# Kernel optimization log

Measured on AMD Instinct MI355X. Metric: run time of the kernel, lower is better.

The kernel has to match this reference:

```python
import jax, jax.numpy as jnp
import numpy as np

D_VOCAB, D_MODEL, N_CTX, D_MLP, D_HEAD, N_HEADS, N_LAYERS = 32000, 1024, 2048, 4096, 64, 16, 4
BATCH, SEQ = 2, 2048


def setup_inputs() -> dict:
    key = jax.random.key(0)
    ks = jax.random.split(key, 12)
    sd = 1.0 / np.sqrt(D_MODEL)
    inp = {
        'tokens': jax.random.randint(ks[0], (BATCH, SEQ), 0, D_VOCAB),
        'W_E': jax.random.normal(ks[1], (D_MODEL, D_VOCAB), jnp.float32) * sd,
        'W_pos': jax.random.normal(ks[2], (N_CTX, D_MODEL), jnp.float32) * sd,
        'W_K': jax.random.normal(ks[3], (N_LAYERS, N_HEADS, D_HEAD, D_MODEL), jnp.float32) * sd,
        'W_Q': jax.random.normal(ks[4], (N_LAYERS, N_HEADS, D_HEAD, D_MODEL), jnp.float32) * sd,
        'W_V': jax.random.normal(ks[5], (N_LAYERS, N_HEADS, D_HEAD, D_MODEL), jnp.float32) * sd,
        'W_O': jax.random.normal(ks[6], (N_LAYERS, D_MODEL, D_HEAD * N_HEADS), jnp.float32) * sd,
        'W_in': jax.random.normal(ks[7], (N_LAYERS, D_MLP, D_MODEL), jnp.float32) * sd,
        'b_in': jnp.zeros((N_LAYERS, D_MLP), jnp.float32),
        'W_out': jax.random.normal(ks[8], (N_LAYERS, D_MODEL, D_MLP), jnp.float32) * sd,
        'b_out': jnp.zeros((N_LAYERS, D_MODEL), jnp.float32),
        'W_U': jax.random.normal(ks[9], (D_MODEL, D_VOCAB), jnp.float32) / np.sqrt(D_VOCAB),
    }
    return inp


def reference(tokens, W_E, W_pos, W_K, W_Q, W_V, W_O, W_in, b_in, W_out, b_out, W_U):
    P = tokens.shape[-1]
    # Embed: einsum('dbp->bpd', W_E[:, x])  ==  W_E.T[tokens]
    x = W_E.T[tokens]                      # [b, p, d]
    x = x + W_pos[:P]                      # PosEmbed
    causal = jnp.tril(jnp.ones((P, P), dtype=bool))  # mask[q, p]: p <= q
    scale = 1.0 / np.sqrt(D_HEAD)
    for l in range(N_LAYERS):
        # --- Attention ---
        k = jnp.einsum('ihd,bpd->biph', W_K[l], x)
        q = jnp.einsum('ihd,bpd->biph', W_Q[l], x)
        v = jnp.einsum('ihd,bpd->biph', W_V[l], x)
        scores = jnp.einsum('biph,biqh->biqp', k, q)
        # tril(scores) - 1e10*(1-mask)  ==  where(mask, scores, -1e10)
        masked = jnp.where(causal, scores, jnp.float32(-1e10))
        attn = jax.nn.softmax(masked * scale, axis=-1)   # softmax over keys p
        z = jnp.einsum('biph,biqp->biqh', v, attn)       # [b, i, q, h]
        z_flat = jnp.transpose(z, (0, 2, 1, 3)).reshape(z.shape[0], P, -1)  # b q (i h)
        attn_out = jnp.einsum('df,bqf->bqd', W_O[l], z_flat)
        x = x + attn_out
        # --- MLP (ReLU) ---
        pre = jnp.einsum('md,bpd->bpm', W_in[l], x) + b_in[l]
        post = jax.nn.relu(pre)
        x = x + jnp.einsum('dm,bpm->bpd', W_out[l], post) + b_out[l]
    return x @ W_U                          # logits [b, p, d_vocab]
```

## Files before the change

### kernel.cpp

```cpp
#include <hip/hip_runtime.h>
#include <hip/hip_bf16.h>
#include <math.h>

#define DV   32000
#define DM   1024
#define DMLP 4096
#define DH   64
#define NH   16
#define NL   4
#define BATCH 2
#define S    2048
#define MTOK (BATCH*S)

typedef __bf16 bf16_t;
typedef bf16_t bf16x8 __attribute__((ext_vector_type(8)));
typedef float  f32x4  __attribute__((ext_vector_type(4)));

#define AS1 __attribute__((address_space(1)))
#define AS3 __attribute__((address_space(3)))

__device__ __forceinline__ void gload16(const bf16_t* g, bf16_t* l) {
    __builtin_amdgcn_global_load_lds((const AS1 void*)g, (AS3 void*)l, 16, 0, 0);
}

__device__ __forceinline__ unsigned short bfbits(float v) {
    union { bf16_t b; unsigned short u; } c; c.b = (bf16_t)v; return c.u;
}
__device__ __forceinline__ float b2f(unsigned short u) {
    union { float f; unsigned v; } c; c.v = ((unsigned)u) << 16; return c.f;
}

template<int MODE, bool BIAS, bool RELU>
__global__ __launch_bounds__(256, 2)
void gemm128d(const bf16_t* __restrict__ A, const bf16_t* __restrict__ Bm,
              char* __restrict__ Out, int ldc,
              const float* __restrict__ bias,
              float* __restrict__ resid, bf16_t* __restrict__ residb,
              int K)
{
    const int mb = blockIdx.x, nb = blockIdx.y;

    __shared__ alignas(16) bf16_t lds[2][2][128*64];

    const int tid  = threadIdx.x;
    const int wave = tid >> 6, lane = tid & 63;
    const int wm = wave >> 1, wn = wave & 1;
    const int l16 = lane & 15, lh = lane >> 4;

    const bf16_t* Abase = A  + (long)(mb*128)*K;
    const bf16_t* Bbase = Bm + (long)(nb*128)*K;

    auto stage2 = [&](int buf, int k0) {
#pragma unroll
        for (int mat=0; mat<2; ++mat) {
            const bf16_t* src = (mat ? Bbase : Abase) + k0;
            bf16_t* dst = &lds[buf][mat][0];
#pragma unroll
            for (int u=0; u<4; ++u) {
                int c = u*256 + tid;
                int row = c >> 3, lc = (c & 7) ^ (row & 7);
                gload16(&src[(long)row*K + lc*8], dst + c*8);
            }
        }
    };

    f32x4 acc[4][4];
#pragma unroll
    for (int i=0;i<4;i++)
#pragma unroll
        for (int j=0;j<4;j++) { f32x4 zv={0.f,0.f,0.f,0.f}; acc[i][j]=zv; }

    const int NT = K >> 6;
    stage2(0, 0);

    int cur = 0;
    for (int kt = 0; kt < NT; ++kt) {
        const int nxt = cur ^ 1;
        const bool more = (kt+1 < NT);

        if (more) {
            stage2(nxt, (kt+1) << 6);
            asm volatile("s_waitcnt vmcnt(8)" ::: "memory");
        } else {
            asm volatile("s_waitcnt vmcnt(0)" ::: "memory");
        }
        asm volatile("s_barrier" ::: "memory");

        bf16x8 af[4][2], bfr[4][2];
#pragma unroll
        for (int i=0;i<4;i++) {
            int ra = wm*64 + i*16 + l16;
#pragma unroll
            for (int kk=0;kk<2;kk++)
                af[i][kk] = *(const bf16x8*)&lds[cur][0][ra*64 + (((kk*4+lh)^(ra&7))*8)];
        }
#pragma unroll
        for (int j=0;j<2;j++) {
            int rb = wn*64 + j*16 + l16;
#pragma unroll
            for (int kk=0;kk<2;kk++)
                bfr[j][kk] = *(const bf16x8*)&lds[cur][1][rb*64 + (((kk*4+lh)^(rb&7))*8)];
        }
        __builtin_amdgcn_s_setprio(1);
#pragma unroll
        for (int kk=0;kk<2;kk++)
#pragma unroll
            for (int i=0;i<4;i++)
#pragma unroll
                for (int j=0;j<2;j++)
                    acc[i][j] = __builtin_amdgcn_mfma_f32_16x16x32_bf16(af[i][kk], bfr[j][kk], acc[i][j], 0,0,0);
        __builtin_amdgcn_s_setprio(0);

#pragma unroll
        for (int j=2;j<4;j++) {
            int rb = wn*64 + j*16 + l16;
#pragma unroll
            for (int kk=0;kk<2;kk++)
                bfr[j][kk] = *(const bf16x8*)&lds[cur][1][rb*64 + (((kk*4+lh)^(rb&7))*8)];
        }
        __builtin_amdgcn_s_setprio(1);
#pragma unroll
        for (int kk=0;kk<2;kk++)
#pragma unroll
            for (int i=0;i<4;i++)
#pragma unroll
                for (int j=2;j<4;j++)
                    acc[i][j] = __builtin_amdgcn_mfma_f32_16x16x32_bf16(af[i][kk], bfr[j][kk], acc[i][j], 0,0,0);
        __builtin_amdgcn_s_setprio(0);

        asm volatile("s_barrier" ::: "memory");
        cur = nxt;
    }

    if constexpr (MODE == 1) {
        float* lsl = reinterpret_cast<float*>(&lds[0][0][0]) + wave*(32*68);
        const int lrow = lane >> 4;
        const int lcq  = lane & 15;
#pragma unroll
        for (int ch=0; ch<2; ++ch) {
#pragma unroll
            for (int il=0; il<2; ++il)
#pragma unroll
                for (int j=0;j<4;j++)
#pragma unroll
                    for (int r=0;r<4;r++)
                        lsl[(il*16 + lh*4 + r)*68 + j*16 + l16] = acc[ch*2+il][j][r];
#pragma unroll
            for (int u=0; u<8; ++u) {
                int rl = u*4 + lrow;
                f32x4 v = *(const f32x4*)&lsl[rl*68 + lcq*4];
                long row = mb*128 + wm*64 + ch*32 + rl;
                long col = nb*128 + wn*64 + lcq*4;
                __builtin_nontemporal_store(v, (f32x4*)&((float*)Out)[row*ldc + col]);
            }
        }
    } else {
#pragma unroll
        for (int i=0;i<4;i++) {
            int row0 = mb*128 + wm*64 + i*16 + lh*4;
#pragma unroll
            for (int j=0;j<4;j++) {
                int col = nb*128 + wn*64 + j*16 + l16;
                float bv = BIAS ? bias[col] : 0.0f;
#pragma unroll
                for (int r=0;r<4;r++) {
                    int row = row0 + r;
                    float v = acc[i][j][r] + bv;
                    if (RELU) v = v > 0.f ? v : 0.f;
                    if constexpr (MODE == 0) {
                        ((bf16_t*)Out)[(long)row*ldc + col] = (bf16_t)v;
                    } else {
                        long o2 = (long)row*ldc + col;
                        float nv = resid[o2] + v;
                        resid[o2]  = nv;
                        residb[o2] = (bf16_t)nv;
                    }
                }
            }
        }
    }
}

template<int MODE, bool BIAS, bool RELU>
__global__ __launch_bounds__(512, 1)
void gemm256(const bf16_t* __restrict__ A, const bf16_t* __restrict__ Bm,
             char* __restrict__ Out, int ldc,
             const float* __restrict__ bias, int K)
{
    const int mb = blockIdx.x, nb = blockIdx.y;

    __shared__ alignas(16) bf16_t lds[2][2][2][128*64];

    const int tid  = threadIdx.x;
    const int wave = tid >> 6, lane = tid & 63;
    const int wm = wave >> 2, wn = wave & 3;
    const int l16 = lane & 15, lh = lane >> 4;

    const bf16_t* Abase = A  + (long)(mb*256)*K;
    const bf16_t* Bbase = Bm + (long)(nb*256)*K;

    const int c0 = tid,       r0 = c0 >> 3, lc0 = (c0 & 7) ^ (r0 & 7);
    const int c1 = 512 + tid, r1 = c1 >> 3, lc1 = (c1 & 7) ^ (r1 & 7);

    auto stage4 = [&](int buf, int k0) {
#pragma unroll
        for (int mat=0; mat<2; ++mat)
#pragma unroll
            for (int half=0; half<2; ++half) {
                const bf16_t* src = (mat ? Bbase : Abase) + (long)(half*128)*K + k0;
                bf16_t* dst = &lds[buf][mat][half][0];
                gload16(&src[(long)r0*K + lc0*8], dst + c0*8);
                gload16(&src[(long)r1*K + lc1*8], dst + c1*8);
            }
    };

    f32x4 acc[8][4];
#pragma unroll
    for (int i=0;i<8;i++)
#pragma unroll
        for (int j=0;j<4;j++) { f32x4 zv={0.f,0.f,0.f,0.f}; acc[i][j]=zv; }

    const int NT = K >> 6;
    stage4(0, 0);

    int cur = 0;
    for (int kt = 0; kt < NT; ++kt) {
        const int nxt = cur ^ 1;
        const bool more = (kt+1 < NT);

        if (more) {
            stage4(nxt, (kt+1) << 6);
            asm volatile("s_waitcnt vmcnt(8)" ::: "memory");
        } else {
            asm volatile("s_waitcnt vmcnt(0)" ::: "memory");
        }
        asm volatile("s_barrier" ::: "memory");

        bf16x8 af[4][2], bfr[4][2];
#pragma unroll
        for (int i=0;i<4;i++) {
            int ra = i*16 + l16;
#pragma unroll
            for (int kk=0;kk<2;kk++)
                af[i][kk] = *(const bf16x8*)&lds[cur][0][wm][ra*64 + (((kk*4+lh)^(ra&7))*8)];
        }
#pragma unroll
        for (int j=0;j<2;j++) {
            int rb = (wn&1)*64 + j*16 + l16;
#pragma unroll
            for (int kk=0;kk<2;kk++)
                bfr[j][kk] = *(const bf16x8*)&lds[cur][1][wn>>1][rb*64 + (((kk*4+lh)^(rb&7))*8)];
        }
        __builtin_amdgcn_s_setprio(1);
#pragma unroll
        for (int kk=0;kk<2;kk++)
#pragma unroll
            for (int i=0;i<4;i++)
#pragma unroll
                for (int j=0;j<2;j++)
                    acc[i][j] = __builtin_amdgcn_mfma_f32_16x16x32_bf16(af[i][kk], bfr[j][kk], acc[i][j], 0,0,0);
        __builtin_amdgcn_s_setprio(0);

#pragma unroll
        for (int j=2;j<4;j++) {
            int rb = (wn&1)*64 + j*16 + l16;
#pragma unroll
            for (int kk=0;kk<2;kk++)
                bfr[j][kk] = *(const bf16x8*)&lds[cur][1][wn>>1][rb*64 + (((kk*4+lh)^(rb&7))*8)];
        }
        __builtin_amdgcn_s_setprio(1);
#pragma unroll
        for (int kk=0;kk<2;kk++)
#pragma unroll
            for (int i=0;i<4;i++)
#pragma unroll
                for (int j=2;j<4;j++)
                    acc[i][j] = __builtin_amdgcn_mfma_f32_16x16x32_bf16(af[i][kk], bfr[j][kk], acc[i][j], 0,0,0);
        __builtin_amdgcn_s_setprio(0);

#pragma unroll
        for (int i=0;i<4;i++) {
            int ra = (i+4)*16 + l16;
#pragma unroll
            for (int kk=0;kk<2;kk++)
                af[i][kk] = *(const bf16x8*)&lds[cur][0][wm][ra*64 + (((kk*4+lh)^(ra&7))*8)];
        }
        __builtin_amdgcn_s_setprio(1);
#pragma unroll
        for (int kk=0;kk<2;kk++)
#pragma unroll
            for (int i=0;i<4;i++)
#pragma unroll
                for (int j=0;j<2;j++)
                    acc[i+4][j] = __builtin_amdgcn_mfma_f32_16x16x32_bf16(af[i][kk], bfr[j][kk], acc[i+4][j], 0,0,0);
        __builtin_amdgcn_s_setprio(0);

        __builtin_amdgcn_s_setprio(1);
#pragma unroll
        for (int kk=0;kk<2;kk++)
#pragma unroll
            for (int i=0;i<4;i++)
#pragma unroll
                for (int j=2;j<4;j++)
                    acc[i+4][j] = __builtin_amdgcn_mfma_f32_16x16x32_bf16(af[i][kk], bfr[j][kk], acc[i+4][j], 0,0,0);
        __builtin_amdgcn_s_setprio(0);

        asm volatile("s_barrier" ::: "memory");
        cur = nxt;
    }

    if constexpr (MODE == 1) {
        float* lsl = reinterpret_cast<float*>(&lds[0][0][0][0]) + wave*(32*68);
        const int lrow = lane >> 4;
        const int lcq  = lane & 15;
#pragma unroll
        for (int ch=0; ch<4; ++ch) {
#pragma unroll
            for (int il=0; il<2; ++il)
#pragma unroll
                for (int j=0;j<4;j++)
#pragma unroll
                    for (int r=0;r<4;r++)
                        lsl[(il*16 + lh*4 + r)*68 + j*16 + l16] = acc[ch*2+il][j][r];
#pragma unroll
            for (int u=0; u<8; ++u) {
                int rl = u*4 + lrow;
                f32x4 v = *(const f32x4*)&lsl[rl*68 + lcq*4];
                long row = mb*256 + wm*128 + ch*32 + rl;
                long col = nb*256 + wn*64 + lcq*4;
                __builtin_nontemporal_store(v, (f32x4*)&((float*)Out)[row*ldc + col]);
            }
        }
    } else {
#pragma unroll
        for (int i=0;i<8;i++) {
            int row0 = mb*256 + wm*128 + i*16 + lh*4;
#pragma unroll
            for (int j=0;j<4;j++) {
                int col = nb*256 + wn*64 + j*16 + l16;
                float bv = BIAS ? bias[col] : 0.0f;
#pragma unroll
                for (int r=0;r<4;r++) {
                    int row = row0 + r;
                    float v = acc[i][j][r] + bv;
                    if (RELU) v = v > 0.f ? v : 0.f;
                    ((bf16_t*)Out)[(long)row*ldc + col] = (bf16_t)v;
                }
            }
        }
    }
}

__global__ __launch_bounds__(256)
void flash_attn(const bf16_t* __restrict__ qkvf,
                const bf16_t* __restrict__ vtg,
                bf16_t* __restrict__ zf)
{
    const int bh = blockIdx.y;
    const int b  = bh >> 4, hd = bh & 15;

    __shared__ alignas(16) bf16_t Kl[2][64*64];
    __shared__ alignas(16) bf16_t Vtl[2][64*64];
    __shared__ alignas(16) bf16_t Pl[4*32*64];

    const int tid = threadIdx.x;
    const int wave = tid >> 6, lane = tid & 63;
    const int l16 = lane & 15, lh = lane >> 4;
    bf16_t* Pw = Pl + wave*32*64;

    auto stageKV = [&](int buf, int kv0) {
#pragma unroll
        for (int u=0; u<2; ++u) {
            int c = u*256 + tid;
            int row = c >> 3, lc = (c & 7) ^ (row & 7);
            gload16(&qkvf[((long)b*S + kv0 + row)*3072 + 1024 + hd*64 + lc*8], &Kl[buf][c*8]);
        }
#pragma unroll
        for (int u=0; u<2; ++u) {
            int c = u*256 + tid;
            int row = c >> 3, lc = (c & 7) ^ (row & 7);
            gload16(&vtg[((long)bh*DH + row)*S + kv0 + lc*8], &Vtl[buf][c*8]);
        }
    };

    const float C = 0.125f;

#pragma unroll 1
    for (int pass = 0; pass < 2; ++pass) {
        const int qt = pass == 0 ? (int)blockIdx.x : 15 - (int)blockIdx.x;
        const int wq_lo = qt*128 + wave*32;

        bf16x8 qr[2][2];
#pragma unroll
        for (int qf=0; qf<2; qf++) {
            int qg = wq_lo + qf*16 + l16;
#pragma unroll
            for (int dhh=0; dhh<2; dhh++)
                qr[qf][dhh] = *(const bf16x8*)&qkvf[((long)b*S + qg)*3072 + hd*64 + dhh*32 + lh*8];
        }

        f32x4 o[4][2];
#pragma unroll
        for (int d=0; d<4; d++)
#pragma unroll
            for (int qf=0; qf<2; qf++) { f32x4 zv={0.f,0.f,0.f,0.f}; o[d][qf]=zv; }
        float mrun[2] = {-1e30f, -1e30f};
        float lrun[2] = {0.f, 0.f};

        const int nt = 2*(qt+1);

        __syncthreads();
        stageKV(0, 0);
        int cur = 0;
        for (int t = 0; t < nt; ++t) {
            const int nxt = cur ^ 1;
            const bool more = (t+1 < nt);
            if (more) {
                stageKV(nxt, (t+1)*64);
                asm volatile("s_waitcnt vmcnt(4)" ::: "memory");
            } else {
                asm volatile("s_waitcnt vmcnt(0)" ::: "memory");
            }
            asm volatile("s_barrier" ::: "memory");

            const int kv0 = t*64;
            f32x4 s[4][2];
#pragma unroll
            for (int f=0; f<4; f++)
#pragma unroll
                for (int qf=0; qf<2; qf++) { f32x4 zv={0.f,0.f,0.f,0.f}; s[f][qf]=zv; }
            __builtin_amdgcn_s_setprio(1);
#pragma unroll
            for (int f=0; f<4; f++) {
                int krow = f*16 + l16;
#pragma unroll
                for (int dhh=0; dhh<2; dhh++) {
                    bf16x8 kfr = *(const bf16x8*)&Kl[cur][krow*64 + (((dhh*4+lh) ^ (krow&7))*8)];
#pragma unroll
                    for (int qf=0; qf<2; qf++)
                        s[f][qf] = __builtin_amdgcn_mfma_f32_16x16x32_bf16(kfr, qr[qf][dhh], s[f][qf], 0,0,0);
                }
            }
            __builtin_amdgcn_s_setprio(0);

            const bool needmask = (kv0 + 64 > wq_lo);

#pragma unroll
            for (int qf=0; qf<2; qf++) {
                int qg = wq_lo + qf*16 + l16;
                float pmax = -1e30f;
#pragma unroll
                for (int f=0; f<4; f++)
#pragma unroll
                    for (int r=0; r<4; r++) {
                        float sv = s[f][qf][r];
                        if (needmask && (kv0 + f*16 + lh*4 + r > qg)) { sv = -1e30f; s[f][qf][r] = sv; }
                        pmax = fmaxf(pmax, sv);
                    }
                pmax = fmaxf(pmax, __shfl_xor(pmax, 16));
                pmax = fmaxf(pmax, __shfl_xor(pmax, 32));
                float mnew = fmaxf(mrun[qf], pmax);
                float corr = __expf((mrun[qf] - mnew)*C);
                mrun[qf] = mnew;
                lrun[qf] *= corr;
#pragma unroll
                for (int d=0; d<4; d++) o[d][qf] *= corr;
                float lsum = 0.f;
                int qloc = qf*16 + l16;
#pragma unroll
                for (int f=0; f<4; f++) {
                    ushort4 pk;
                    float p0 = __expf((s[f][qf][0]-mnew)*C);
                    float p1 = __expf((s[f][qf][1]-mnew)*C);
                    float p2 = __expf((s[f][qf][2]-mnew)*C);
                    float p3 = __expf((s[f][qf][3]-mnew)*C);
                    lsum += (p0+p1) + (p2+p3);
                    pk.x = bfbits(p0); pk.y = bfbits(p1); pk.z = bfbits(p2); pk.w = bfbits(p3);
                    int phys = (f*2 + (lh>>1)) ^ (qloc & 7);
                    *(ushort4*)&Pw[qloc*64 + phys*8 + (lh&1)*4] = pk;
                }
                lrun[qf] += lsum;
            }

#pragma unroll
            for (int kh=0; kh<2; kh++) {
                bf16x8 pb[2];
#pragma unroll
                for (int qf=0; qf<2; qf++) {
                    int qloc = qf*16 + l16;
                    pb[qf] = *(const bf16x8*)&Pw[qloc*64 + (((kh*4+lh) ^ (qloc&7))*8)];
                }
                __builtin_amdgcn_s_setprio(1);
#pragma unroll
                for (int d=0; d<4; d++) {
                    int vrow = d*16 + l16;
                    bf16x8 va = *(const bf16x8*)&Vtl[cur][vrow*64 + (((kh*4+lh) ^ (vrow&7))*8)];
#pragma unroll
                    for (int qf=0; qf<2; qf++)
                        o[d][qf] = __builtin_amdgcn_mfma_f32_16x16x32_bf16(va, pb[qf], o[d][qf], 0,0,0);
                }
                __builtin_amdgcn_s_setprio(0);
            }
            asm volatile("s_barrier" ::: "memory");
            cur = nxt;
        }

#pragma unroll
        for (int qf=0; qf<2; qf++) {
            float lt = lrun[qf];
            lt += __shfl_xor(lt, 16);
            lt += __shfl_xor(lt, 32);
            float inv = 1.0f / lt;
            int qg = wq_lo + qf*16 + l16;
#pragma unroll
            for (int d=0; d<4; d++) {
                ushort4 ov;
                ov.x = bfbits(o[d][qf][0]*inv);
                ov.y = bfbits(o[d][qf][1]*inv);
                ov.z = bfbits(o[d][qf][2]*inv);
                ov.w = bfbits(o[d][qf][3]*inv);
                *(ushort4*)&zf[((long)b*S + qg)*DM + hd*64 + d*16 + lh*4] = ov;
            }
        }
    }
}

__global__ __launch_bounds__(256) void k_conv_qkv(
    const float* __restrict__ Wq, const float* __restrict__ Wk,
    const float* __restrict__ Wv, bf16_t* __restrict__ out)
{
    long idx = ((long)blockIdx.x*256 + threadIdx.x)*4;
    long l = idx / (3072L*DM);
    long r = idx % (3072L*DM);
    int row = (int)(r / DM), d = (int)(r % DM);
    int sel = row >> 10, rr = row & 1023;
    const float* src = sel==0 ? Wq : (sel==1 ? Wk : Wv);
    float4 v = *(const float4*)&src[(l*1024 + rr)*(long)DM + d];
    ushort4 o;
    o.x = bfbits(v.x); o.y = bfbits(v.y); o.z = bfbits(v.z); o.w = bfbits(v.w);
    *(ushort4*)&out[idx] = o;
}

__global__ __launch_bounds__(256) void k_conv(const float* __restrict__ src,
                                              bf16_t* __restrict__ dst, long n)
{
    long i = ((long)blockIdx.x*256 + threadIdx.x)*4;
    if (i >= n) return;
    float4 v = *(const float4*)&src[i];
    ushort4 o;
    o.x = bfbits(v.x); o.y = bfbits(v.y); o.z = bfbits(v.z); o.w = bfbits(v.w);
    *(ushort4*)&dst[i] = o;
}

__global__ __launch_bounds__(256) void k_trans(const float* __restrict__ W,
                                               bf16_t* __restrict__ out, int NC)
{
    __shared__ float tile[32][33];
    int n0 = blockIdx.x*32, k0 = blockIdx.y*32;
    int tx = threadIdx.x & 31, ty = threadIdx.x >> 5;
#pragma unroll
    for (int u=0;u<4;u++)
        tile[ty+u*8][tx] = W[(long)(k0+ty+u*8)*NC + n0+tx];
    __syncthreads();
#pragma unroll
    for (int u=0;u<4;u++)
        out[(long)(n0+ty+u*8)*DM + k0+tx] = (bf16_t)tile[tx][ty+u*8];
}

__global__ __launch_bounds__(256) void k_embed(const int* __restrict__ tok,
    const bf16_t* __restrict__ WEt, const float* __restrict__ Wpos,
    float* __restrict__ xf, bf16_t* __restrict__ xb)
{
    int bp = blockIdx.x;
    int p  = bp & (S-1);
    int t  = tok[bp];
    int d  = threadIdx.x*4;
    ushort4 e = *(const ushort4*)&WEt[(long)t*DM + d];
    float4  w = *(const float4*)&Wpos[(long)p*DM + d];
    float4 v;
    v.x = b2f(e.x)+w.x; v.y = b2f(e.y)+w.y; v.z = b2f(e.z)+w.z; v.w = b2f(e.w)+w.w;
    *(float4*)&xf[(long)bp*DM + d] = v;
    ushort4 o;
    o.x = bfbits(v.x); o.y = bfbits(v.y); o.z = bfbits(v.z); o.w = bfbits(v.w);
    *(ushort4*)&xb[(long)bp*DM + d] = o;
}

__global__ __launch_bounds__(256) void k_permv(const bf16_t* __restrict__ qkv,
    bf16_t* __restrict__ vt)
{
    __shared__ bf16_t tile[64][66];
    const int p0 = blockIdx.x*64;
    const int bh = blockIdx.y;
    const int b  = bh >> 4, hd = bh & 15;
    const int tx = threadIdx.x & 63, ty = threadIdx.x >> 6;
#pragma unroll
    for (int u=0;u<16;u++) {
        int r = u*4 + ty;
        tile[r][tx] = qkv[((long)b*S + p0 + r)*3072 + 2048 + hd*64 + tx];
    }
    __syncthreads();
#pragma unroll
    for (int u=0;u<16;u++) {
        int hh = u*4 + ty;
        vt[(((long)bh)*DH + hh)*S + p0 + tx] = tile[tx][hh];
    }
}

extern "C" void kernel_launch(void* const* d_in, const int* in_sizes, int n_in,
                              void* d_out, int out_size, void* d_ws, size_t ws_size,
                              hipStream_t stream)
{
    const int*   tokens = (const int*)d_in[0];
    const float* W_E    = (const float*)d_in[1];
    const float* W_pos  = (const float*)d_in[2];
    const float* W_K    = (const float*)d_in[3];
    const float* W_Q    = (const float*)d_in[4];
    const float* W_V    = (const float*)d_in[5];
    const float* W_O    = (const float*)d_in[6];
    const float* W_in   = (const float*)d_in[7];
    const float* b_in   = (const float*)d_in[8];
    const float* W_out  = (const float*)d_in[9];
    const float* b_out  = (const float*)d_in[10];
    const float* W_U    = (const float*)d_in[11];
    float* out = (float*)d_out;

    char* ws = (char*)d_ws;
    long off = 0;
    auto alloc = [&](long bytes)->char* {
        char* p = ws + off; off += (bytes + 255) & ~255L; return p;
    };
    bf16_t* wqkv = (bf16_t*)alloc((long)NL*3072*DM*2);
    bf16_t* wo   = (bf16_t*)alloc((long)NL*DM*DM*2);
    bf16_t* win  = (bf16_t*)alloc((long)NL*DMLP*DM*2);
    bf16_t* wout = (bf16_t*)alloc((long)NL*DM*DMLP*2);
    bf16_t* wut  = (bf16_t*)alloc((long)DV*DM*2);
    bf16_t* wet  = (bf16_t*)alloc((long)DV*DM*2);
    float*  xf   = (float*)alloc((long)MTOK*DM*4);
    bf16_t* xb   = (bf16_t*)alloc((long)MTOK*DM*2);
    bf16_t* qkvf = (bf16_t*)alloc((long)MTOK*3072*2);
    bf16_t* vt   = (bf16_t*)alloc((long)BATCH*NH*S*DH*2);
    bf16_t* zf   = (bf16_t*)alloc((long)MTOK*DM*2);
    bf16_t* post = (bf16_t*)alloc((long)MTOK*DMLP*2);

    k_conv_qkv<<<(int)(((long)NL*3072*DM)/1024), 256, 0, stream>>>(W_Q, W_K, W_V, wqkv);
    k_conv<<<(int)(((long)NL*DM*DM)/1024),   256, 0, stream>>>(W_O,   wo,   (long)NL*DM*DM);
    k_conv<<<(int)(((long)NL*DMLP*DM)/1024), 256, 0, stream>>>(W_in,  win,  (long)NL*DMLP*DM);
    k_conv<<<(int)(((long)NL*DM*DMLP)/1024), 256, 0, stream>>>(W_out, wout, (long)NL*DM*DMLP);
    k_trans<<<dim3(DV/32, DM/32), 256, 0, stream>>>(W_U, wut, DV);
    k_trans<<<dim3(DV/32, DM/32), 256, 0, stream>>>(W_E, wet, DV);

    k_embed<<<MTOK, 256, 0, stream>>>(tokens, wet, W_pos, xf, xb);

    for (int l = 0; l < NL; ++l) {
        gemm128d<0,false,false><<<dim3(MTOK/128, 3072/128), 256, 0, stream>>>(
            xb, wqkv + (long)l*3072*DM, (char*)qkvf, 3072, nullptr, nullptr, nullptr, DM);
        k_permv<<<dim3(S/64, BATCH*NH), 256, 0, stream>>>(qkvf, vt);

        flash_attn<<<dim3(S/256, BATCH*NH), 256, 0, stream>>>(qkvf, vt, zf);

        gemm128d<2,false,false><<<dim3(MTOK/128, DM/128), 256, 0, stream>>>(
            zf, wo + (long)l*DM*DM, nullptr, DM, nullptr, xf, xb, DM);
        gemm128d<0,true,true><<<dim3(MTOK/128, DMLP/128), 256, 0, stream>>>(
            xb, win + (long)l*DMLP*DM, (char*)post, DMLP,
            b_in + (long)l*DMLP, nullptr, nullptr, DM);
        gemm128d<2,true,false><<<dim3(MTOK/128, DM/128), 256, 0, stream>>>(
            post, wout + (long)l*DM*DMLP, nullptr, DM,
            b_out + (long)l*DM, xf, xb, DMLP);
    }

    gemm256<1,false,false><<<dim3(MTOK/256, DV/256), 512, 0, stream>>>(
        xb, wut, (char*)out, DV, nullptr, DM);
}
```

Before: 1.425 ms.

## Make unembed GEMM persistent with cross-tile prefetch of next tile's operands

The final vocab-projection GEMM now launches 256 persistent blocks that loop over output tiles in M-major order. The first K-slice of a block's next tile is staged into the spare LDS buffer during the last K-step of the current tile, so loads overlap the epilogue. The fp32 epilogue now stages one 16-row slab per wave through the idle LDS buffer. This adds a __syncthreads per tile and changes the tile visiting order, which affects L2 reuse of the weight and activation panels.

```diff
diff --git a/kernel.cpp b/kernel.cpp
--- a/kernel.cpp
+++ b/kernel.cpp
@@ -185,10 +185,8 @@
 __global__ __launch_bounds__(512, 1)
 void gemm256(const bf16_t* __restrict__ A, const bf16_t* __restrict__ Bm,
              char* __restrict__ Out, int ldc,
-             const float* __restrict__ bias, int K)
-{
-    const int mb = blockIdx.x, nb = blockIdx.y;
-
+             const float* __restrict__ bias, int K, int mbn, int ntiles)
+{
     __shared__ alignas(16) bf16_t lds[2][2][2][128*64];
 
     const int tid  = threadIdx.x;
@@ -196,158 +194,169 @@
     const int wm = wave >> 2, wn = wave & 3;
     const int l16 = lane & 15, lh = lane >> 4;
 
-    const bf16_t* Abase = A  + (long)(mb*256)*K;
-    const bf16_t* Bbase = Bm + (long)(nb*256)*K;
-
     const int c0 = tid,       r0 = c0 >> 3, lc0 = (c0 & 7) ^ (r0 & 7);
     const int c1 = 512 + tid, r1 = c1 >> 3, lc1 = (c1 & 7) ^ (r1 & 7);
 
-    auto stage4 = [&](int buf, int k0) {
+    auto stage4 = [&](int buf, const bf16_t* Ab, const bf16_t* Bb, int k0) {
 #pragma unroll
         for (int mat=0; mat<2; ++mat)
 #pragma unroll
             for (int half=0; half<2; ++half) {
-                const bf16_t* src = (mat ? Bbase : Abase) + (long)(half*128)*K + k0;
+                const bf16_t* src = (mat ? Bb : Ab) + (long)(half*128)*K + k0;
                 bf16_t* dst = &lds[buf][mat][half][0];
                 gload16(&src[(long)r0*K + lc0*8], dst + c0*8);
                 gload16(&src[(long)r1*K + lc1*8], dst + c1*8);
             }
     };
 
-    f32x4 acc[8][4];
-#pragma unroll
-    for (int i=0;i<8;i++)
-#pragma unroll
-        for (int j=0;j<4;j++) { f32x4 zv={0.f,0.f,0.f,0.f}; acc[i][j]=zv; }
-
     const int NT = K >> 6;
-    stage4(0, 0);
-
     int cur = 0;
-    for (int kt = 0; kt < NT; ++kt) {
-        const int nxt = cur ^ 1;
-        const bool more = (kt+1 < NT);
-
-        if (more) {
-            stage4(nxt, (kt+1) << 6);
-            asm volatile("s_waitcnt vmcnt(8)" ::: "memory");
+    bool first = true;
+
+    for (int t = blockIdx.x; t < ntiles; t += gridDim.x) {
+        const int mb = t % mbn, nb = t / mbn;
+        const bf16_t* Ab = A  + (long)(mb*256)*K;
+        const bf16_t* Bb = Bm + (long)(nb*256)*K;
+        const int t2 = t + gridDim.x;
+        const bf16_t* Ab2 = nullptr; const bf16_t* Bb2 = nullptr;
+        if (t2 < ntiles) {
+            Ab2 = A  + (long)((t2 % mbn)*256)*K;
+            Bb2 = Bm + (long)((t2 / mbn)*256)*K;
+        }
+
+        if (first) { stage4(cur, Ab, Bb, 0); first = false; }
+
+        f32x4 acc[8][4];
+#pragma unroll
+        for (int i=0;i<8;i++)
+#pragma unroll
+            for (int j=0;j<4;j++) { f32x4 zv={0.f,0.f,0.f,0.f}; acc[i][j]=zv; }
+
+        for (int kt = 0; kt < NT; ++kt) {
+            const int nxt = cur ^ 1;
+            const bool inner = (kt+1 < NT);
+
+            if (inner) {
+                stage4(nxt, Ab, Bb, (kt+1) << 6);
+                asm volatile("s_waitcnt vmcnt(8)" ::: "memory");
+            } else if (Ab2) {
+                stage4(nxt, Ab2, Bb2, 0);
+                asm volatile("s_waitcnt vmcnt(8)" ::: "memory");
+            } else {
+                asm volatile("s_waitcnt vmcnt(0)" ::: "memory");
+            }
+            asm volatile("s_barrier" ::: "memory");
+
+            bf16x8 af[4][2], bfr[4][2];
+#pragma unroll
+            for (int i=0;i<4;i++) {
+                int ra = i*16 + l16;
+#pragma unroll
+                for (int kk=0;kk<2;kk++)
+                    af[i][kk] = *(const bf16x8*)&lds[cur][0][wm][ra*64 + (((kk*4+lh)^(ra&7))*8)];
+            }
+#pragma unroll
+            for (int j=0;j<2;j++) {
+                int rb = (wn&1)*64 + j*16 + l16;
+#pragma unroll
+                for (int kk=0;kk<2;kk++)
+                    bfr[j][kk] = *(const bf16x8*)&lds[cur][1][wn>>1][rb*64 + (((kk*4+lh)^(rb&7))*8)];
+            }
+            __builtin_amdgcn_s_setprio(1);
+#pragma unroll
+            for (int kk=0;kk<2;kk++)
+#pragma unroll
+                for (int i=0;i<4;i++)
+#pragma unroll
+                    for (int j=0;j<2;j++)
+                        acc[i][j] = __builtin_amdgcn_mfma_f32_16x16x32_bf16(af[i][kk], bfr[j][kk], acc[i][j], 0,0,0);
+            __builtin_amdgcn_s_setprio(0);
+
+#pragma unroll
+            for (int j=2;j<4;j++) {
+                int rb = (wn&1)*64 + j*16 + l16;
+#pragma unroll
+                for (int kk=0;kk<2;kk++)
+                    bfr[j][kk] = *(const bf16x8*)&lds[cur][1][wn>>1][rb*64 + (((kk*4+lh)^(rb&7))*8)];
+            }
+            __builtin_amdgcn_s_setprio(1);
+#pragma unroll
+            for (int kk=0;kk<2;kk++)
+#pragma unroll
+                for (int i=0;i<4;i++)
+#pragma unroll
+                    for (int j=2;j<4;j++)
+                        acc[i][j] = __builtin_amdgcn_mfma_f32_16x16x32_bf16(af[i][kk], bfr[j][kk], acc[i][j], 0,0,0);
+            __builtin_amdgcn_s_setprio(0);
+
+#pragma unroll
+            for (int i=0;i<4;i++) {
+                int ra = (i+4)*16 + l16;
+#pragma unroll
+                for (int kk=0;kk<2;kk++)
+                    af[i][kk] = *(const bf16x8*)&lds[cur][0][wm][ra*64 + (((kk*4+lh)^(ra&7))*8)];
+            }
+            __builtin_amdgcn_s_setprio(1);
+#pragma unroll
+            for (int kk=0;kk<2;kk++)
+#pragma unroll
+                for (int i=0;i<4;i++)
+#pragma unroll
+                    for (int j=0;j<2;j++)
+                        acc[i+4][j] = __builtin_amdgcn_mfma_f32_16x16x32_bf16(af[i][kk], bfr[j][kk], acc[i+4][j], 0,0,0);
+
+#pragma unroll
+            for (int kk=0;kk<2;kk++)
+#pragma unroll
+                for (int i=0;i<4;i++)
+#pragma unroll
+                    for (int j=2;j<4;j++)
+                        acc[i+4][j] = __builtin_amdgcn_mfma_f32_16x16x32_bf16(af[i][kk], bfr[j][kk], acc[i+4][j], 0,0,0);
+            __builtin_amdgcn_s_setprio(0);
+
+            asm volatile("s_barrier" ::: "memory");
+            cur = nxt;
+        }
+
+        if constexpr (MODE == 1) {
+            float* lsl = reinterpret_cast<float*>(&lds[cur^1][0][0][0]) + wave*(16*68);
+            const int lrow = lane >> 4;
+            const int lcq  = lane & 15;
+#pragma unroll
+            for (int i=0;i<8;i++) {
+#pragma unroll
+                for (int j=0;j<4;j++)
+#pragma unroll
+                    for (int r=0;r<4;r++)
+                        lsl[(lh*4 + r)*68 + j*16 + l16] = acc[i][j][r];
+#pragma unroll
+                for (int u=0; u<4; ++u) {
+                    int rl = u*4 + lrow;
+                    f32x4 v = *(const f32x4*)&lsl[rl*68 + lcq*4];
+                    long row = mb*256 + wm*128 + i*16 + rl;
+                    long col = nb*256 + wn*64 + lcq*4;
+                    __builtin_nontemporal_store(v, (f32x4*)&((float*)Out)[row*ldc + col]);
+                }
+            }
         } else {
-            asm volatile("s_waitcnt vmcnt(0)" ::: "memory");
-        }
-        asm volatile("s_barrier" ::: "memory");
-
-        bf16x8 af[4][2], bfr[4][2];
-#pragma unroll
-        for (int i=0;i<4;i++) {
-            int ra = i*16 + l16;
-#pragma unroll
-            for (int kk=0;kk<2;kk++)
-                af[i][kk] = *(const bf16x8*)&lds[cur][0][wm][ra*64 + (((kk*4+lh)^(ra&7))*8)];
-        }
-#pragma unroll
-        for (int j=0;j<2;j++) {
-            int rb = (wn&1)*64 + j*16 + l16;
-#pragma unroll
-            for (int kk=0;kk<2;kk++)
-                bfr[j][kk] = *(const bf16x8*)&lds[cur][1][wn>>1][rb*64 + (((kk*4+lh)^(rb&7))*8)];
-        }
-        __builtin_amdgcn_s_setprio(1);
-#pragma unroll
-        for (int kk=0;kk<2;kk++)
-#pragma unroll
-            for (int i=0;i<4;i++)
-#pragma unroll
-                for (int j=0;j<2;j++)
-                    acc[i][j] = __builtin_amdgcn_mfma_f32_16x16x32_bf16(af[i][kk], bfr[j][kk], acc[i][j], 0,0,0);
-        __builtin_amdgcn_s_setprio(0);
-
-#pragma unroll
-        for (int j=2;j<4;j++) {
-            int rb = (wn&1)*64 + j*16 + l16;
-#pragma unroll
-            for (int kk=0;kk<2;kk++)
-                bfr[j][kk] = *(const bf16x8*)&lds[cur][1][wn>>1][rb*64 + (((kk*4+lh)^(rb&7))*8)];
-        }
-        __builtin_amdgcn_s_setprio(1);
-#pragma unroll
-        for (int kk=0;kk<2;kk++)
-#pragma unroll
-            for (int i=0;i<4;i++)
-#pragma unroll
-                for (int j=2;j<4;j++)
-                    acc[i][j] = __builtin_amdgcn_mfma_f32_16x16x32_bf16(af[i][kk], bfr[j][kk], acc[i][j], 0,0,0);
-        __builtin_amdgcn_s_setprio(0);
-
-#pragma unroll
-        for (int i=0;i<4;i++) {
-            int ra = (i+4)*16 + l16;
-#pragma unroll
-            for (int kk=0;kk<2;kk++)
-                af[i][kk] = *(const bf16x8*)&lds[cur][0][wm][ra*64 + (((kk*4+lh)^(ra&7))*8)];
-        }
-        __builtin_amdgcn_s_setprio(1);
-#pragma unroll
-        for (int kk=0;kk<2;kk++)
-#pragma unroll
-            for (int i=0;i<4;i++)
-#pragma unroll
-                for (int j=0;j<2;j++)
-                    acc[i+4][j] = __builtin_amdgcn_mfma_f32_16x16x32_bf16(af[i][kk], bfr[j][kk], acc[i+4][j], 0,0,0);
-        __builtin_amdgcn_s_setprio(0);
-
-        __builtin_amdgcn_s_setprio(1);
-#pragma unroll
-        for (int kk=0;kk<2;kk++)
-#pragma unroll
-            for (int i=0;i<4;i++)
-#pragma unroll
-                for (int j=2;j<4;j++)
-                    acc[i+4][j] = __builtin_amdgcn_mfma_f32_16x16x32_bf16(af[i][kk], bfr[j][kk], acc[i+4][j], 0,0,0);
-        __builtin_amdgcn_s_setprio(0);
-
-        asm volatile("s_barrier" ::: "memory");
-        cur = nxt;
-    }
-
-    if constexpr (MODE == 1) {
-        float* lsl = reinterpret_cast<float*>(&lds[0][0][0][0]) + wave*(32*68);
-        const int lrow = lane >> 4;
-        const int lcq  = lane & 15;
-#pragma unroll
-        for (int ch=0; ch<4; ++ch) {
-#pragma unroll
-            for (int il=0; il<2; ++il)
-#pragma unroll
-                for (int j=0;j<4;j++)
-#pragma unroll
-                    for (int r=0;r<4;r++)
-                        lsl[(il*16 + lh*4 + r)*68 + j*16 + l16] = acc[ch*2+il][j][r];
-#pragma unroll
-            for (int u=0; u<8; ++u) {
-                int rl = u*4 + lrow;
-                f32x4 v = *(const f32x4*)&lsl[rl*68 + lcq*4];
-                long row = mb*256 + wm*128 + ch*32 + rl;
-                long col = nb*256 + wn*64 + lcq*4;
-                __builtin_nontemporal_store(v, (f32x4*)&((float*)Out)[row*ldc + col]);
-            }
-        }
-    } else {
-#pragma unroll
-        for (int i=0;i<8;i++) {
-            int row0 = mb*256 + wm*128 + i*16 + lh*4;
-#pragma unroll
-            for (int j=0;j<4;j++) {
-                int col = nb*256 + wn*64 + j*16 + l16;
-                float bv = BIAS ? bias[col] : 0.0f;
-#pragma unroll
-                for (int r=0;r<4;r++) {
-                    int row = row0 + r;
-                    float v = acc[i][j][r] + bv;
-                    if (RELU) v = v > 0.f ? v : 0.f;
-                    ((bf16_t*)Out)[(long)row*ldc + col] = (bf16_t)v;
+#pragma unroll
+            for (int i=0;i<8;i++) {
+                int row0 = mb*256 + wm*128 + i*16 + lh*4;
+#pragma unroll
+                for (int j=0;j<4;j++) {
+                    int col = nb*256 + wn*64 + j*16 + l16;
+                    float bv = BIAS ? bias[col] : 0.0f;
+#pragma unroll
+                    for (int r=0;r<4;r++) {
+                        int row = row0 + r;
+                        float v = acc[i][j][r] + bv;
+                        if (RELU) v = v > 0.f ? v : 0.f;
+                        ((bf16_t*)Out)[(long)row*ldc + col] = (bf16_t)v;
+                    }
                 }
             }
         }
+        __syncthreads();
     }
 }
 
@@ -668,6 +677,6 @@
             b_out + (long)l*DM, xf, xb, DMLP);
     }
 
-    gemm256<1,false,false><<<dim3(MTOK/256, DV/256), 512, 0, stream>>>(
-        xb, wut, (char*)out, DV, nullptr, DM);
-}
+    gemm256<1,false,false><<<256, 512, 0, stream>>>(
+        xb, wut, (char*)out, DV, nullptr, DM, MTOK/256, (MTOK/256)*(DV/256));
+}
```

Measured after the change: 1.425 ms. Within noise of the previous version (-0.0%).

## Interleave next-tile global-to-LDS loads across MFMA phases in GEMM main loop

Applied to the files above, without the earlier changes.

Splits the per-iteration staging of the next K tile into four quarter-loads, each issued between MFMA compute phases. Explicit lgkmcnt waits, sched_barriers and extra s_barriers pin the ordering. The goal is to spread global-memory traffic across the compute and hide load latency behind the MFMAs. In exchange it adds several workgroup barriers per iteration and holds separate A-fragment registers, which raises register pressure.

```diff
diff --git a/kernel.cpp b/kernel.cpp
--- a/kernel.cpp
+++ b/kernel.cpp
@@ -202,16 +202,11 @@
     const int c0 = tid,       r0 = c0 >> 3, lc0 = (c0 & 7) ^ (r0 & 7);
     const int c1 = 512 + tid, r1 = c1 >> 3, lc1 = (c1 & 7) ^ (r1 & 7);
 
-    auto stage4 = [&](int buf, int k0) {
-#pragma unroll
-        for (int mat=0; mat<2; ++mat)
-#pragma unroll
-            for (int half=0; half<2; ++half) {
-                const bf16_t* src = (mat ? Bbase : Abase) + (long)(half*128)*K + k0;
-                bf16_t* dst = &lds[buf][mat][half][0];
-                gload16(&src[(long)r0*K + lc0*8], dst + c0*8);
-                gload16(&src[(long)r1*K + lc1*8], dst + c1*8);
-            }
+    auto stageHalf = [&](int buf, int mat, int half, int k0) {
+        const bf16_t* src = (mat ? Bbase : Abase) + (long)(half*128)*K + k0;
+        bf16_t* dst = &lds[buf][mat][half][0];
+        gload16(&src[(long)r0*K + lc0*8], dst + c0*8);
+        gload16(&src[(long)r1*K + lc1*8], dst + c1*8);
     };
 
     f32x4 acc[8][4];
@@ -221,28 +216,30 @@
         for (int j=0;j<4;j++) { f32x4 zv={0.f,0.f,0.f,0.f}; acc[i][j]=zv; }
 
     const int NT = K >> 6;
-    stage4(0, 0);
+    stageHalf(0,0,0,0); stageHalf(0,0,1,0); stageHalf(0,1,0,0); stageHalf(0,1,1,0);
+    asm volatile("s_waitcnt vmcnt(0)" ::: "memory");
+    asm volatile("s_barrier" ::: "memory");
 
     int cur = 0;
     for (int kt = 0; kt < NT; ++kt) {
         const int nxt = cur ^ 1;
+        const int k1 = (kt+1) << 6;
         const bool more = (kt+1 < NT);
 
-        if (more) {
-            stage4(nxt, (kt+1) << 6);
-            asm volatile("s_waitcnt vmcnt(8)" ::: "memory");
-        } else {
-            asm volatile("s_waitcnt vmcnt(0)" ::: "memory");
+        bf16x8 af0[4][2], af1[4][2], bfr[4][2];
+
+        if (more) stageHalf(nxt,0,0,k1);
+        if (kt > 0) {
+            if (more) { asm volatile("s_waitcnt vmcnt(2)" ::: "memory"); }
+            else      { asm volatile("s_waitcnt vmcnt(0)" ::: "memory"); }
         }
         asm volatile("s_barrier" ::: "memory");
-
-        bf16x8 af[4][2], bfr[4][2];
 #pragma unroll
         for (int i=0;i<4;i++) {
             int ra = i*16 + l16;
 #pragma unroll
             for (int kk=0;kk<2;kk++)
-                af[i][kk] = *(const bf16x8*)&lds[cur][0][wm][ra*64 + (((kk*4+lh)^(ra&7))*8)];
+                af0[i][kk] = *(const bf16x8*)&lds[cur][0][wm][ra*64 + (((kk*4+lh)^(ra&7))*8)];
         }
 #pragma unroll
         for (int j=0;j<2;j++) {
@@ -251,6 +248,8 @@
             for (int kk=0;kk<2;kk++)
                 bfr[j][kk] = *(const bf16x8*)&lds[cur][1][wn>>1][rb*64 + (((kk*4+lh)^(rb&7))*8)];
         }
+        asm volatile("s_waitcnt lgkmcnt(0)" ::: "memory");
+        __builtin_amdgcn_sched_barrier(0);
         __builtin_amdgcn_s_setprio(1);
 #pragma unroll
         for (int kk=0;kk<2;kk++)
@@ -258,8 +257,9 @@
             for (int i=0;i<4;i++)
 #pragma unroll
                 for (int j=0;j<2;j++)
-                    acc[i][j] = __builtin_amdgcn_mfma_f32_16x16x32_bf16(af[i][kk], bfr[j][kk], acc[i][j], 0,0,0);
+                    acc[i][j] = __builtin_amdgcn_mfma_f32_16x16x32_bf16(af0[i][kk], bfr[j][kk], acc[i][j], 0,0,0);
         __builtin_amdgcn_s_setprio(0);
+        asm volatile("s_barrier" ::: "memory");
 
 #pragma unroll
         for (int j=2;j<4;j++) {
@@ -268,6 +268,9 @@
             for (int kk=0;kk<2;kk++)
                 bfr[j][kk] = *(const bf16x8*)&lds[cur][1][wn>>1][rb*64 + (((kk*4+lh)^(rb&7))*8)];
         }
+        if (more) stageHalf(nxt,0,1,k1);
+        asm volatile("s_waitcnt lgkmcnt(0)" ::: "memory");
+        __builtin_amdgcn_sched_barrier(0);
         __builtin_amdgcn_s_setprio(1);
 #pragma unroll
         for (int kk=0;kk<2;kk++)
@@ -275,16 +278,20 @@
             for (int i=0;i<4;i++)
 #pragma unroll
                 for (int j=2;j<4;j++)
-                    acc[i][j] = __builtin_amdgcn_mfma_f32_16x16x32_bf16(af[i][kk], bfr[j][kk], acc[i][j], 0,0,0);
+                    acc[i][j] = __builtin_amdgcn_mfma_f32_16x16x32_bf16(af0[i][kk], bfr[j][kk], acc[i][j], 0,0,0);
         __builtin_amdgcn_s_setprio(0);
+        asm volatile("s_barrier" ::: "memory");
 
 #pragma unroll
         for (int i=0;i<4;i++) {
             int ra = (i+4)*16 + l16;
 #pragma unroll
             for (int kk=0;kk<2;kk++)
-                af[i][kk] = *(const bf16x8*)&lds[cur][0][wm][ra*64 + (((kk*4+lh)^(ra&7))*8)];
-        }
+                af1[i][kk] = *(const bf16x8*)&lds[cur][0][wm][ra*64 + (((kk*4+lh)^(ra&7))*8)];
+        }
+        if (more) stageHalf(nxt,1,0,k1);
+        asm volatile("s_waitcnt lgkmcnt(0)" ::: "memory");
+        __builtin_amdgcn_sched_barrier(0);
         __builtin_amdgcn_s_setprio(1);
 #pragma unroll
         for (int kk=0;kk<2;kk++)
@@ -292,9 +299,11 @@
             for (int i=0;i<4;i++)
 #pragma unroll
                 for (int j=0;j<2;j++)
-                    acc[i+4][j] = __builtin_amdgcn_mfma_f32_16x16x32_bf16(af[i][kk], bfr[j][kk], acc[i+4][j], 0,0,0);
+                    acc[i+4][j] = __builtin_amdgcn_mfma_f32_16x16x32_bf16(af1[i][kk], bfr[j][kk], acc[i+4][j], 0,0,0);
         __builtin_amdgcn_s_setprio(0);
-
+        asm volatile("s_barrier" ::: "memory");
+
+        if (more) stageHalf(nxt,1,1,k1);
         __builtin_amdgcn_s_setprio(1);
 #pragma unroll
         for (int kk=0;kk<2;kk++)
@@ -302,9 +311,8 @@
             for (int i=0;i<4;i++)
 #pragma unroll
                 for (int j=2;j<4;j++)
-                    acc[i+4][j] = __builtin_amdgcn_mfma_f32_16x16x32_bf16(af[i][kk], bfr[j][kk], acc[i+4][j], 0,0,0);
+                    acc[i+4][j] = __builtin_amdgcn_mfma_f32_16x16x32_bf16(af1[i][kk], bfr[j][kk], acc[i+4][j], 0,0,0);
         __builtin_amdgcn_s_setprio(0);
-
         asm volatile("s_barrier" ::: "memory");
         cur = nxt;
     }
```

Result: no change. 1.451 ms (+1.8%).
